# Kernel tuning notes

Measured on AMD Instinct MI355X. Metric: run time of the kernel, lower is better.

## Reference

```python
import jax, jax.numpy as jnp
import numpy as np

D_MODEL = 512
NUM_HEADS = 8
D_K = D_MODEL // NUM_HEADS


def setup_inputs() -> dict:
    key = jax.random.key(0)
    ks = jax.random.split(key, 9)
    B, N = 4, 2048
    x = jax.random.normal(ks[0], (B, N, D_MODEL), dtype=jnp.float32)
    s = 1.0 / np.sqrt(D_MODEL)
    Wq = jax.random.normal(ks[1], (D_MODEL, D_MODEL), dtype=jnp.float32) * s
    bq = jax.random.normal(ks[2], (D_MODEL,), dtype=jnp.float32) * 0.02
    Wk = jax.random.normal(ks[3], (D_MODEL, D_MODEL), dtype=jnp.float32) * s
    bk = jax.random.normal(ks[4], (D_MODEL,), dtype=jnp.float32) * 0.02
    Wv = jax.random.normal(ks[5], (D_MODEL, D_MODEL), dtype=jnp.float32) * s
    bv = jax.random.normal(ks[6], (D_MODEL,), dtype=jnp.float32) * 0.02
    Wo = jax.random.normal(ks[7], (D_MODEL, D_MODEL), dtype=jnp.float32) * s
    bo = jax.random.normal(ks[8], (D_MODEL,), dtype=jnp.float32) * 0.02
    return {"x": x, "Wq": Wq, "bq": bq, "Wk": Wk, "bk": bk,
            "Wv": Wv, "bv": bv, "Wo": Wo, "bo": bo}


def reference(x, Wq, bq, Wk, bk, Wv, bv, Wo, bo):
    B, N, _ = x.shape
    # project and split heads: [B, H, N, d_k]
    def split_heads(t):
        return t.reshape(B, N, NUM_HEADS, D_K).transpose(0, 2, 1, 3)
    Q = split_heads(x @ Wq + bq)
    K = split_heads(x @ Wk + bk)
    V = split_heads(x @ Wv + bv)
    scale = 1.0 / np.sqrt(D_K)
    scores = jnp.einsum('bhqd,bhkd->bhqk', Q, K) * scale  # [B,H,N,N]
    probs = jax.nn.softmax(scores, axis=-1)
    attn = jnp.einsum('bhqk,bhkd->bhqd', probs, V)
    attn = attn.transpose(0, 2, 1, 3).reshape(B, N, D_MODEL)
    return attn @ Wo + bo
```

## Files before the change

kernel.cpp:

```cpp
#include <hip/hip_runtime.h>
#include <math.h>

#define D_MODEL 512
#define N_SEQ   2048
#define H       8
#define DK      64

typedef __attribute__((ext_vector_type(8)))  short bf16x8;
typedef __attribute__((ext_vector_type(4)))  float f32x4;
typedef __attribute__((ext_vector_type(16))) float f32x16;

__device__ __forceinline__ unsigned short f2b(float f) {
    unsigned int u = __float_as_uint(f);
    u += 0x7FFF + ((u >> 16) & 1);
    return (unsigned short)(u >> 16);
}

__device__ __forceinline__ unsigned int pack2(float lo, float hi) {
#if __has_builtin(__builtin_amdgcn_cvt_pk_bf16_f32)
    typedef __attribute__((ext_vector_type(2))) short bf16x2;
    bf16x2 p = __builtin_amdgcn_cvt_pk_bf16_f32(lo, hi);
    return (unsigned int)(unsigned short)p[0] |
           ((unsigned int)(unsigned short)p[1] << 16);
#else
    return (unsigned int)f2b(lo) | ((unsigned int)f2b(hi) << 16);
#endif
}

__device__ __forceinline__ float fexp2(float x) {
#if __has_builtin(__builtin_amdgcn_exp2f)
    return __builtin_amdgcn_exp2f(x);
#else
    return __expf(x * 0.6931471805599453f);
#endif
}

#define SC2 0.18033688011112042f

__global__ void convert_bf16(const float* __restrict__ in,
                             unsigned short* __restrict__ out)
{
    const int i = (blockIdx.x * 256 + threadIdx.x) * 8;
    float4 a = *(const float4*)(in + i);
    float4 b = *(const float4*)(in + i + 4);
    unsigned int w[4];
    w[0] = pack2(a.x, a.y); w[1] = pack2(a.z, a.w);
    w[2] = pack2(b.x, b.y); w[3] = pack2(b.z, b.w);
    *(bf16x8*)(out + i) = *(bf16x8*)w;
}

__global__ void transpose_all(
    const float* __restrict__ W0, const float* __restrict__ W1,
    const float* __restrict__ W2, const float* __restrict__ W3,
    unsigned short* __restrict__ T0, unsigned short* __restrict__ T1,
    unsigned short* __restrict__ T2, unsigned short* __restrict__ T3)
{
    const float* W; unsigned short* Wt;
    if      (blockIdx.z == 0) { W = W0; Wt = T0; }
    else if (blockIdx.z == 1) { W = W1; Wt = T1; }
    else if (blockIdx.z == 2) { W = W2; Wt = T2; }
    else                      { W = W3; Wt = T3; }

    __shared__ float t[32][33];
    const int tx = threadIdx.x, ty = threadIdx.y;
    const int x = blockIdx.x * 32 + tx;
    const int y0 = blockIdx.y * 32;
    for (int i = ty; i < 32; i += 8)
        t[i][tx] = W[(size_t)(y0 + i) * D_MODEL + x];
    __syncthreads();
    const int ox = blockIdx.y * 32 + tx;
    const int oy0 = blockIdx.x * 32;
    for (int i = ty; i < 32; i += 8)
        Wt[(size_t)(oy0 + i) * D_MODEL + ox] = f2b(t[tx][i]);
}

__global__ __launch_bounds__(256, 4) void gemm_qkv(
    const unsigned short* __restrict__ xb,
    const unsigned short* __restrict__ Wtq,
    const unsigned short* __restrict__ Wtk,
    const unsigned short* __restrict__ Wtv,
    const float* __restrict__ bq, const float* __restrict__ bk,
    const float* __restrict__ bv,
    unsigned short* __restrict__ Qb, unsigned short* __restrict__ Kb,
    unsigned short* __restrict__ Vtb)
{
    __shared__ unsigned short As[128][72];
    __shared__ unsigned short Bs[64][72];

    const unsigned short* Wt; const float* bias; unsigned short* out; int isV;
    float sc;
    if (blockIdx.z == 0)      { Wt = Wtq; bias = bq; out = Qb;  isV = 0; sc = SC2; }
    else if (blockIdx.z == 1) { Wt = Wtk; bias = bk; out = Kb;  isV = 0; sc = 1.0f; }
    else                      { Wt = Wtv; bias = bv; out = Vtb; isV = 1; sc = 1.0f; }

    const int tid  = threadIdx.x;
    const int lane = tid & 63, wave = tid >> 6;
    const int m0 = blockIdx.y * 128, n0 = blockIdx.x * 64;
    const int wm = (wave & 1) * 64, wn = (wave >> 1) * 32;
    const int cn = lane & 15, g = lane >> 4;

    const int arow = tid >> 1, acol = (tid & 1) * 32;
    const int brow = tid >> 2, bcol = (tid & 3) * 16;
    const unsigned short* Ag = xb + (size_t)(m0 + arow) * D_MODEL + acol;
    const unsigned short* Bg = Wt + (size_t)(n0 + brow) * D_MODEL + bcol;

    f32x4 acc[4][2];
    #pragma unroll
    for (int i = 0; i < 4; ++i)
        #pragma unroll
        for (int j = 0; j < 2; ++j)
            acc[i][j] = (f32x4){0.f, 0.f, 0.f, 0.f};

    for (int k0 = 0; k0 < D_MODEL; k0 += 64) {
        bf16x8 av[4], bv2[2];
        #pragma unroll
        for (int q = 0; q < 4; ++q) av[q] = *(const bf16x8*)(Ag + k0 + q * 8);
        #pragma unroll
        for (int q = 0; q < 2; ++q) bv2[q] = *(const bf16x8*)(Bg + k0 + q * 8);
        __syncthreads();
        #pragma unroll
        for (int q = 0; q < 4; ++q) *(bf16x8*)&As[arow][acol + q * 8] = av[q];
        #pragma unroll
        for (int q = 0; q < 2; ++q) *(bf16x8*)&Bs[brow][bcol + q * 8] = bv2[q];
        __syncthreads();

        #pragma unroll
        for (int ks = 0; ks < 2; ++ks) {
            bf16x8 af[4], bf[2];
            #pragma unroll
            for (int i = 0; i < 4; ++i)
                af[i] = *(const bf16x8*)&As[wm + i * 16 + cn][ks * 32 + g * 8];
            #pragma unroll
            for (int j = 0; j < 2; ++j)
                bf[j] = *(const bf16x8*)&Bs[wn + j * 16 + cn][ks * 32 + g * 8];
            if (!isV) {
                #pragma unroll
                for (int i = 0; i < 4; ++i)
                    #pragma unroll
                    for (int j = 0; j < 2; ++j)
                        acc[i][j] = __builtin_amdgcn_mfma_f32_16x16x32_bf16(
                            bf[j], af[i], acc[i][j], 0, 0, 0);
            } else {
                #pragma unroll
                for (int i = 0; i < 4; ++i)
                    #pragma unroll
                    for (int j = 0; j < 2; ++j)
                        acc[i][j] = __builtin_amdgcn_mfma_f32_16x16x32_bf16(
                            af[i], bf[j], acc[i][j], 0, 0, 0);
            }
        }
    }

    if (!isV) {
        #pragma unroll
        for (int j = 0; j < 2; ++j) {
            const int dbase = n0 + wn + j * 16 + g * 4;
            const int hh = dbase >> 6, dd = dbase & 63;
            float4 bb = *(const float4*)&bias[dbase];
            #pragma unroll
            for (int i = 0; i < 4; ++i) {
                const int tt = m0 + wm + i * 16 + cn;
                const int bi = tt >> 11, tok = tt & (N_SEQ - 1);
                ushort4 pk;
                pk.x = f2b((acc[i][j][0] + bb.x) * sc);
                pk.y = f2b((acc[i][j][1] + bb.y) * sc);
                pk.z = f2b((acc[i][j][2] + bb.z) * sc);
                pk.w = f2b((acc[i][j][3] + bb.w) * sc);
                *(ushort4*)(out + (((size_t)bi * H + hh) * N_SEQ + tok) * DK + dd) = pk;
            }
        }
    } else {
        #pragma unroll
        for (int j = 0; j < 2; ++j) {
            const int n = n0 + wn + j * 16 + cn;
            const int hh = n >> 6, dd = n & 63;
            const float bb = bias[n];
            #pragma unroll
            for (int i = 0; i < 4; ++i) {
                const int m = m0 + wm + i * 16 + g * 4;
                const int bi = m >> 11, t = m & (N_SEQ - 1);
                ushort4 pk;
                pk.x = f2b(acc[i][j][0] + bb);
                pk.y = f2b(acc[i][j][1] + bb);
                pk.z = f2b(acc[i][j][2] + bb);
                pk.w = f2b(acc[i][j][3] + bb);
                *(ushort4*)(out + (((size_t)bi * H + hh) * DK + dd) * N_SEQ + t) = pk;
            }
        }
    }
}

__global__ __launch_bounds__(256, 4) void gemm_o(
    const unsigned short* __restrict__ A,
    const unsigned short* __restrict__ Wt,
    const float* __restrict__ bias, float* __restrict__ out)
{
    __shared__ unsigned short As[64][72];
    __shared__ unsigned short Bs[64][72];

    const int tid  = threadIdx.x;
    const int lane = tid & 63, wave = tid >> 6;
    const int m0 = blockIdx.y * 64, n0 = blockIdx.x * 64;
    const int wm = (wave & 1) * 32, wn = (wave >> 1) * 32;
    const int cn = lane & 15, g = lane >> 4;

    const int srow = tid >> 2;
    const int scol = (tid & 3) * 16;
    const unsigned short* Ag = A  + (size_t)(m0 + srow) * D_MODEL + scol;
    const unsigned short* Bg = Wt + (size_t)(n0 + srow) * D_MODEL + scol;

    f32x4 acc[2][2];
    #pragma unroll
    for (int i = 0; i < 2; ++i)
        #pragma unroll
        for (int j = 0; j < 2; ++j)
            acc[i][j] = (f32x4){0.f, 0.f, 0.f, 0.f};

    for (int k0 = 0; k0 < D_MODEL; k0 += 64) {
        bf16x8 av[2], bv[2];
        #pragma unroll
        for (int q = 0; q < 2; ++q) {
            av[q] = *(const bf16x8*)(Ag + k0 + q * 8);
            bv[q] = *(const bf16x8*)(Bg + k0 + q * 8);
        }
        __syncthreads();
        #pragma unroll
        for (int q = 0; q < 2; ++q) {
            *(bf16x8*)&As[srow][scol + q * 8] = av[q];
            *(bf16x8*)&Bs[srow][scol + q * 8] = bv[q];
        }
        __syncthreads();

        #pragma unroll
        for (int ks = 0; ks < 2; ++ks) {
            bf16x8 af[2], bf[2];
            #pragma unroll
            for (int i = 0; i < 2; ++i)
                af[i] = *(const bf16x8*)&As[wm + i * 16 + cn][ks * 32 + g * 8];
            #pragma unroll
            for (int j = 0; j < 2; ++j)
                bf[j] = *(const bf16x8*)&Bs[wn + j * 16 + cn][ks * 32 + g * 8];
            #pragma unroll
            for (int i = 0; i < 2; ++i)
                #pragma unroll
                for (int j = 0; j < 2; ++j)
                    acc[i][j] = __builtin_amdgcn_mfma_f32_16x16x32_bf16(
                        af[i], bf[j], acc[i][j], 0, 0, 0);
        }
    }

    #pragma unroll
    for (int j = 0; j < 2; ++j) {
        const int n = n0 + wn + j * 16 + cn;
        const float bb = bias[n];
        #pragma unroll
        for (int i = 0; i < 2; ++i)
            #pragma unroll
            for (int r = 0; r < 4; ++r) {
                const int m = m0 + wm + i * 16 + g * 4 + r;
                out[(size_t)m * D_MODEL + n] = acc[i][j][r] + bb;
            }
    }
}

__global__ __launch_bounds__(256, 2) void attn_mfma(
    const unsigned short* __restrict__ Q,
    const unsigned short* __restrict__ K,
    const unsigned short* __restrict__ Vt,
    unsigned short* __restrict__ ctx)
{
    __shared__ unsigned short SM[2][2][64][72];

    const int bid = blockIdx.x;
    const int qt = (bid >> 3) & 15;
    const int bh = (bid & 7) * 4 + (bid >> 7);
    const int b = bh >> 3, h = bh & 7;

    const int tid = threadIdx.x, lane = tid & 63, wave = tid >> 6;
    const int sp = wave >> 1;
    const int w4 = wave & 1;
    const int lq = lane & 31, hf = lane >> 5;
    const int qbase = qt * 128 + w4 * 64;

    const size_t hb = (size_t)b * H + h;
    const unsigned short* Qp = Q  + hb * N_SEQ * DK;
    const unsigned short* Kp = K  + hb * N_SEQ * DK;
    const unsigned short* Vp = Vt + hb * DK * N_SEQ;

    bf16x8 qf[2][4];
    #pragma unroll
    for (int u = 0; u < 2; ++u)
        #pragma unroll
        for (int kd = 0; kd < 4; ++kd)
            qf[u][kd] = *(const bf16x8*)(Qp +
                (size_t)(qbase + u * 32 + lq) * DK + kd * 16 + hf * 8);

    f32x16 O[2][2], Ol[2];
    #pragma unroll
    for (int u = 0; u < 2; ++u)
        #pragma unroll
        for (int r = 0; r < 16; ++r) {
            O[u][0][r] = 0.f; O[u][1][r] = 0.f; Ol[u][r] = 0.f;
        }

    bf16x8 onesA;
    {
        const short v = (lq == 0) ? (short)0x3F80 : (short)0;
        #pragma unroll
        for (int j = 0; j < 8; ++j) onesA[j] = v;
    }

    const int sps = tid >> 7;
    const int tl = tid & 127;
    const int krow = tl >> 1, kcol = (tl & 1) * 32;
    unsigned short (*Kss)[72] = SM[sps][0];
    unsigned short (*Vss)[72] = SM[sps][1];
    unsigned short (*Ks)[72]  = SM[sp][0];
    unsigned short (*Vs)[72]  = SM[sp][1];

    for (int it = 0; it < 16; ++it) {
        const int j0 = sps * (N_SEQ / 2) + it * 64;
        bf16x8 kv[4], vv[4];
        #pragma unroll
        for (int q = 0; q < 4; ++q) {
            kv[q] = *(const bf16x8*)(Kp + (size_t)(j0 + krow) * DK + kcol + q * 8);
            vv[q] = *(const bf16x8*)(Vp + (size_t)krow * N_SEQ + j0 + kcol + q * 8);
        }
        bf16x8 sw[4];
        {
            ushort4* v0 = (ushort4*)&vv[0]; ushort4* v1 = (ushort4*)&vv[1];
            ushort4* v2 = (ushort4*)&vv[2]; ushort4* v3 = (ushort4*)&vv[3];
            ushort4* s0 = (ushort4*)&sw[0]; ushort4* s1 = (ushort4*)&sw[1];
            ushort4* s2 = (ushort4*)&sw[2]; ushort4* s3 = (ushort4*)&sw[3];
            s0[0] = v0[0]; s0[1] = v1[0];
            s1[0] = v0[1]; s1[1] = v1[1];
            s2[0] = v2[0]; s2[1] = v3[0];
            s3[0] = v2[1]; s3[1] = v3[1];
        }
        __syncthreads();
        #pragma unroll
        for (int q = 0; q < 4; ++q) {
            *(bf16x8*)&Kss[krow][kcol + q * 8] = kv[q];
            *(bf16x8*)&Vss[krow][kcol + q * 8] = sw[q];
        }
        __syncthreads();

        bf16x8 ka0[4], ka1[4];
        #pragma unroll
        for (int kd = 0; kd < 4; ++kd) {
            ka0[kd] = *(const bf16x8*)&Ks[lq][kd * 16 + hf * 8];
            ka1[kd] = *(const bf16x8*)&Ks[32 + lq][kd * 16 + hf * 8];
        }

        unsigned int pA[2][4][2], pB[2][4][2];
        #pragma unroll
        for (int u = 0; u < 2; ++u) {
            f32x16 s0, s1;
            #pragma unroll
            for (int r = 0; r < 16; ++r) { s0[r] = 0.f; s1[r] = 0.f; }
            #pragma unroll
            for (int kd = 0; kd < 4; ++kd) {
                s0 = __builtin_amdgcn_mfma_f32_32x32x16_bf16(ka0[kd], qf[u][kd], s0, 0, 0, 0);
                s1 = __builtin_amdgcn_mfma_f32_32x32x16_bf16(ka1[kd], qf[u][kd], s1, 0, 0, 0);
            }
            #pragma unroll
            for (int c = 0; c < 4; ++c)
                #pragma unroll
                for (int p = 0; p < 2; ++p) {
                    pA[u][c][p] = pack2(fexp2(s0[4 * c + 2 * p]),
                                        fexp2(s0[4 * c + 2 * p + 1]));
                    pB[u][c][p] = pack2(fexp2(s1[4 * c + 2 * p]),
                                        fexp2(s1[4 * c + 2 * p + 1]));
                }
        }

        bf16x8 va0[4], va1[4];
        #pragma unroll
        for (int ks = 0; ks < 4; ++ks) {
            va0[ks] = *(const bf16x8*)&Vs[lq][ks * 16 + hf * 8];
            va1[ks] = *(const bf16x8*)&Vs[32 + lq][ks * 16 + hf * 8];
        }

        #pragma unroll
        for (int u = 0; u < 2; ++u)
            #pragma unroll
            for (int ks = 0; ks < 4; ++ks) {
                const unsigned int (*src)[2] = (ks < 2) ? pA[u] : pB[u];
                const int c2 = (ks & 1) * 2;
                bf16x8 bp;
                unsigned int* bpu = (unsigned int*)&bp;
                bpu[0] = src[c2][0];     bpu[1] = src[c2][1];
                bpu[2] = src[c2 + 1][0]; bpu[3] = src[c2 + 1][1];
                O[u][0] = __builtin_amdgcn_mfma_f32_32x32x16_bf16(va0[ks], bp, O[u][0], 0, 0, 0);
                O[u][1] = __builtin_amdgcn_mfma_f32_32x32x16_bf16(va1[ks], bp, O[u][1], 0, 0, 0);
                Ol[u]   = __builtin_amdgcn_mfma_f32_32x32x16_bf16(onesA,   bp, Ol[u],   0, 0, 0);
            }
    }

    float* R    = (float*)&SM[0][0][0][0];
    float* Laux = R + 2 * 2 * 64 * 32;

    __syncthreads();
    if (sp == 1) {
        #pragma unroll
        for (int u = 0; u < 2; ++u) {
            #pragma unroll
            for (int dt = 0; dt < 2; ++dt)
                #pragma unroll
                for (int r = 0; r < 16; ++r) {
                    const int d = (r & 3) + 8 * (r >> 2) + 4 * hf + 32 * dt;
                    R[(((w4 * 2 + u) * 64) + d) * 32 + lq] = O[u][dt][r];
                }
            if (hf == 0) Laux[(w4 * 2 + u) * 32 + lq] = Ol[u][0];
        }
    }
    __syncthreads();
    if (sp == 0) {
        #pragma unroll
        for (int u = 0; u < 2; ++u) {
            #pragma unroll
            for (int dt = 0; dt < 2; ++dt)
                #pragma unroll
                for (int r = 0; r < 16; ++r) {
                    const int d = (r & 3) + 8 * (r >> 2) + 4 * hf + 32 * dt;
                    O[u][dt][r] += R[(((w4 * 2 + u) * 64) + d) * 32 + lq];
                }
            const float lsum = Ol[u][0] + Laux[(w4 * 2 + u) * 32 + lq];
            const float linv = 1.0f / __shfl(lsum, lq);

            unsigned short* ob = ctx +
                ((size_t)b * N_SEQ + qbase + u * 32 + lq) * D_MODEL
                + h * DK + hf * 4;
            #pragma unroll
            for (int dt = 0; dt < 2; ++dt)
                #pragma unroll
                for (int c = 0; c < 4; ++c) {
                    unsigned int w2[2];
                    w2[0] = pack2(O[u][dt][4 * c + 0] * linv,
                                  O[u][dt][4 * c + 1] * linv);
                    w2[1] = pack2(O[u][dt][4 * c + 2] * linv,
                                  O[u][dt][4 * c + 3] * linv);
                    *(unsigned int*)(ob + dt * 32 + c * 8)     = w2[0];
                    *(unsigned int*)(ob + dt * 32 + c * 8 + 2) = w2[1];
                }
        }
    }
}

extern "C" void kernel_launch(void* const* d_in, const int* in_sizes, int n_in,
                              void* d_out, int out_size, void* d_ws, size_t ws_size,
                              hipStream_t stream)
{
    const float* x  = (const float*)d_in[0];
    const float* Wq = (const float*)d_in[1];
    const float* bq = (const float*)d_in[2];
    const float* Wk = (const float*)d_in[3];
    const float* bk = (const float*)d_in[4];
    const float* Wv = (const float*)d_in[5];
    const float* bv = (const float*)d_in[6];
    const float* Wo = (const float*)d_in[7];
    const float* bo = (const float*)d_in[8];
    float* out = (float*)d_out;

    const int M = in_sizes[0] / D_MODEL;
    const size_t NX = (size_t)M * D_MODEL;
    const size_t NW = (size_t)D_MODEL * D_MODEL;

    unsigned short* xb  = (unsigned short*)d_ws;
    unsigned short* Wtq = xb + NX;
    unsigned short* Wtk = Wtq + NW;
    unsigned short* Wtv = Wtk + NW;
    unsigned short* Wto = Wtv + NW;
    unsigned short* Qb  = Wto + NW;
    unsigned short* Kb  = Qb + NX;
    unsigned short* Vtb = Kb + NX;
    unsigned short* ctx = Vtb + NX;

    convert_bf16<<<NX / (256 * 8), 256, 0, stream>>>(x, xb);
    transpose_all<<<dim3(16, 16, 4), dim3(32, 8), 0, stream>>>(
        Wq, Wk, Wv, Wo, Wtq, Wtk, Wtv, Wto);

    gemm_qkv<<<dim3(D_MODEL / 64, M / 128, 3), 256, 0, stream>>>(
        xb, Wtq, Wtk, Wtv, bq, bk, bv, Qb, Kb, Vtb);
    attn_mfma<<<512, 256, 0, stream>>>(Qb, Kb, Vtb, ctx);
    gemm_o<<<dim3(D_MODEL / 64, M / 64), 256, 0, stream>>>(ctx, Wto, bo, out);
}
```

Before: 179.1 us.

## Drop LDS staging in projection GEMMs, load MFMA fragments directly from global

```diff
diff --git a/kernel.cpp b/kernel.cpp
--- a/kernel.cpp
+++ b/kernel.cpp
@@ -84,76 +84,61 @@
     unsigned short* __restrict__ Qb, unsigned short* __restrict__ Kb,
     unsigned short* __restrict__ Vtb)
 {
-    __shared__ unsigned short As[128][72];
-    __shared__ unsigned short Bs[64][72];
-
-    const unsigned short* Wt; const float* bias; unsigned short* out; int isV;
-    float sc;
-    if (blockIdx.z == 0)      { Wt = Wtq; bias = bq; out = Qb;  isV = 0; sc = SC2; }
-    else if (blockIdx.z == 1) { Wt = Wtk; bias = bk; out = Kb;  isV = 0; sc = 1.0f; }
-    else                      { Wt = Wtv; bias = bv; out = Vtb; isV = 1; sc = 1.0f; }
-
-    const int tid  = threadIdx.x;
-    const int lane = tid & 63, wave = tid >> 6;
-    const int m0 = blockIdx.y * 128, n0 = blockIdx.x * 64;
-    const int wm = (wave & 1) * 64, wn = (wave >> 1) * 32;
+    const int bid = blockIdx.x;
+    const int m0 = ((bid & 7) + 8 * ((bid >> 3) & 7)) * 128;
+    const int nz = bid >> 6;
+    const int n0 = (nz & 3) * 128;
+    const int z  = nz >> 2;
+
+    const unsigned short* Wt; const float* bias; unsigned short* out;
+    float sc; int isV;
+    if (z == 0)      { Wt = Wtq; bias = bq; out = Qb;  sc = SC2;  isV = 0; }
+    else if (z == 1) { Wt = Wtk; bias = bk; out = Kb;  sc = 1.0f; isV = 0; }
+    else             { Wt = Wtv; bias = bv; out = Vtb; sc = 1.0f; isV = 1; }
+
+    const int lane = threadIdx.x & 63, wave = threadIdx.x >> 6;
+    const int wm = (wave & 1) * 64, wn = (wave >> 1) * 64;
     const int cn = lane & 15, g = lane >> 4;
 
-    const int arow = tid >> 1, acol = (tid & 1) * 32;
-    const int brow = tid >> 2, bcol = (tid & 3) * 16;
-    const unsigned short* Ag = xb + (size_t)(m0 + arow) * D_MODEL + acol;
-    const unsigned short* Bg = Wt + (size_t)(n0 + brow) * D_MODEL + bcol;
-
-    f32x4 acc[4][2];
+    const unsigned short* Arow = xb + (size_t)(m0 + wm + cn) * D_MODEL + g * 8;
+    const unsigned short* Brow = Wt + (size_t)(n0 + wn + cn) * D_MODEL + g * 8;
+
+    f32x4 acc[4][4];
     #pragma unroll
     for (int i = 0; i < 4; ++i)
         #pragma unroll
-        for (int j = 0; j < 2; ++j)
+        for (int j = 0; j < 4; ++j)
             acc[i][j] = (f32x4){0.f, 0.f, 0.f, 0.f};
 
-    for (int k0 = 0; k0 < D_MODEL; k0 += 64) {
-        bf16x8 av[4], bv2[2];
-        #pragma unroll
-        for (int q = 0; q < 4; ++q) av[q] = *(const bf16x8*)(Ag + k0 + q * 8);
-        #pragma unroll
-        for (int q = 0; q < 2; ++q) bv2[q] = *(const bf16x8*)(Bg + k0 + q * 8);
-        __syncthreads();
-        #pragma unroll
-        for (int q = 0; q < 4; ++q) *(bf16x8*)&As[arow][acol + q * 8] = av[q];
-        #pragma unroll
-        for (int q = 0; q < 2; ++q) *(bf16x8*)&Bs[brow][bcol + q * 8] = bv2[q];
-        __syncthreads();
-
-        #pragma unroll
-        for (int ks = 0; ks < 2; ++ks) {
-            bf16x8 af[4], bf[2];
+    #pragma unroll 4
+    for (int k0 = 0; k0 < D_MODEL; k0 += 32) {
+        bf16x8 af[4], bf[4];
+        #pragma unroll
+        for (int i = 0; i < 4; ++i)
+            af[i] = *(const bf16x8*)(Arow + (size_t)i * 16 * D_MODEL + k0);
+        #pragma unroll
+        for (int j = 0; j < 4; ++j)
+            bf[j] = *(const bf16x8*)(Brow + (size_t)j * 16 * D_MODEL + k0);
+        if (!isV) {
             #pragma unroll
             for (int i = 0; i < 4; ++i)
-                af[i] = *(const bf16x8*)&As[wm + i * 16 + cn][ks * 32 + g * 8];
-            #pragma unroll
-            for (int j = 0; j < 2; ++j)
-                bf[j] = *(const bf16x8*)&Bs[wn + j * 16 + cn][ks * 32 + g * 8];
-            if (!isV) {
-                #pragma unroll
-                for (int i = 0; i < 4; ++i)
-                    #pragma unroll
-                    for (int j = 0; j < 2; ++j)
-                        acc[i][j] = __builtin_amdgcn_mfma_f32_16x16x32_bf16(
-                            bf[j], af[i], acc[i][j], 0, 0, 0);
-            } else {
-                #pragma unroll
-                for (int i = 0; i < 4; ++i)
-                    #pragma unroll
-                    for (int j = 0; j < 2; ++j)
-                        acc[i][j] = __builtin_amdgcn_mfma_f32_16x16x32_bf16(
-                            af[i], bf[j], acc[i][j], 0, 0, 0);
-            }
+                #pragma unroll
+                for (int j = 0; j < 4; ++j)
+                    acc[i][j] = __builtin_amdgcn_mfma_f32_16x16x32_bf16(
+                        bf[j], af[i], acc[i][j], 0, 0, 0);
+        } else {
+            #pragma unroll
+            for (int i = 0; i < 4; ++i)
+                #pragma unroll
+                for (int j = 0; j < 4; ++j)
+                    acc[i][j] = __builtin_amdgcn_mfma_f32_16x16x32_bf16(
+                        af[i], bf[j], acc[i][j], 0, 0, 0);
         }
     }
 
     if (!isV) {
         #pragma unroll
-        for (int j = 0; j < 2; ++j) {
+        for (int j = 0; j < 4; ++j) {
             const int dbase = n0 + wn + j * 16 + g * 4;
             const int hh = dbase >> 6, dd = dbase & 63;
             float4 bb = *(const float4*)&bias[dbase];
@@ -171,7 +156,7 @@
         }
     } else {
         #pragma unroll
-        for (int j = 0; j < 2; ++j) {
+        for (int j = 0; j < 4; ++j) {
             const int n = n0 + wn + j * 16 + cn;
             const int hh = n >> 6, dd = n & 63;
             const float bb = bias[n];
@@ -195,62 +180,43 @@
     const unsigned short* __restrict__ Wt,
     const float* __restrict__ bias, float* __restrict__ out)
 {
-    __shared__ unsigned short As[64][72];
-    __shared__ unsigned short Bs[64][72];
-
-    const int tid  = threadIdx.x;
-    const int lane = tid & 63, wave = tid >> 6;
-    const int m0 = blockIdx.y * 64, n0 = blockIdx.x * 64;
-    const int wm = (wave & 1) * 32, wn = (wave >> 1) * 32;
+    const int bid = blockIdx.x;
+    const int m0 = ((bid & 7) + 8 * ((bid >> 3) & 15)) * 64;
+    const int n0 = (bid >> 7) * 128;
+
+    const int lane = threadIdx.x & 63, wave = threadIdx.x >> 6;
+    const int wm = (wave & 1) * 32, wn = (wave >> 1) * 64;
     const int cn = lane & 15, g = lane >> 4;
 
-    const int srow = tid >> 2;
-    const int scol = (tid & 3) * 16;
-    const unsigned short* Ag = A  + (size_t)(m0 + srow) * D_MODEL + scol;
-    const unsigned short* Bg = Wt + (size_t)(n0 + srow) * D_MODEL + scol;
-
-    f32x4 acc[2][2];
+    const unsigned short* Arow = A  + (size_t)(m0 + wm + cn) * D_MODEL + g * 8;
+    const unsigned short* Brow = Wt + (size_t)(n0 + wn + cn) * D_MODEL + g * 8;
+
+    f32x4 acc[2][4];
     #pragma unroll
     for (int i = 0; i < 2; ++i)
         #pragma unroll
-        for (int j = 0; j < 2; ++j)
+        for (int j = 0; j < 4; ++j)
             acc[i][j] = (f32x4){0.f, 0.f, 0.f, 0.f};
 
-    for (int k0 = 0; k0 < D_MODEL; k0 += 64) {
-        bf16x8 av[2], bv[2];
-        #pragma unroll
-        for (int q = 0; q < 2; ++q) {
-            av[q] = *(const bf16x8*)(Ag + k0 + q * 8);
-            bv[q] = *(const bf16x8*)(Bg + k0 + q * 8);
-        }
-        __syncthreads();
-        #pragma unroll
-        for (int q = 0; q < 2; ++q) {
-            *(bf16x8*)&As[srow][scol + q * 8] = av[q];
-            *(bf16x8*)&Bs[srow][scol + q * 8] = bv[q];
-        }
-        __syncthreads();
-
-        #pragma unroll
-        for (int ks = 0; ks < 2; ++ks) {
-            bf16x8 af[2], bf[2];
-            #pragma unroll
-            for (int i = 0; i < 2; ++i)
-                af[i] = *(const bf16x8*)&As[wm + i * 16 + cn][ks * 32 + g * 8];
-            #pragma unroll
-            for (int j = 0; j < 2; ++j)
-                bf[j] = *(const bf16x8*)&Bs[wn + j * 16 + cn][ks * 32 + g * 8];
-            #pragma unroll
-            for (int i = 0; i < 2; ++i)
-                #pragma unroll
-                for (int j = 0; j < 2; ++j)
-                    acc[i][j] = __builtin_amdgcn_mfma_f32_16x16x32_bf16(
-                        af[i], bf[j], acc[i][j], 0, 0, 0);
-        }
+    #pragma unroll 4
+    for (int k0 = 0; k0 < D_MODEL; k0 += 32) {
+        bf16x8 af[2], bf[4];
+        #pragma unroll
+        for (int i = 0; i < 2; ++i)
+            af[i] = *(const bf16x8*)(Arow + (size_t)i * 16 * D_MODEL + k0);
+        #pragma unroll
+        for (int j = 0; j < 4; ++j)
+            bf[j] = *(const bf16x8*)(Brow + (size_t)j * 16 * D_MODEL + k0);
+        #pragma unroll
+        for (int i = 0; i < 2; ++i)
+            #pragma unroll
+            for (int j = 0; j < 4; ++j)
+                acc[i][j] = __builtin_amdgcn_mfma_f32_16x16x32_bf16(
+                    af[i], bf[j], acc[i][j], 0, 0, 0);
     }
 
     #pragma unroll
-    for (int j = 0; j < 2; ++j) {
+    for (int j = 0; j < 4; ++j) {
         const int n = n0 + wn + j * 16 + cn;
         const float bb = bias[n];
         #pragma unroll
@@ -480,8 +446,8 @@
     transpose_all<<<dim3(16, 16, 4), dim3(32, 8), 0, stream>>>(
         Wq, Wk, Wv, Wo, Wtq, Wtk, Wtv, Wto);
 
-    gemm_qkv<<<dim3(D_MODEL / 64, M / 128, 3), 256, 0, stream>>>(
+    gemm_qkv<<<768, 256, 0, stream>>>(
         xb, Wtq, Wtk, Wtv, bq, bk, bv, Qb, Kb, Vtb);
     attn_mfma<<<512, 256, 0, stream>>>(Qb, Kb, Vtb, ctx);
-    gemm_o<<<dim3(D_MODEL / 64, M / 64), 256, 0, stream>>>(ctx, Wto, bo, out);
-}
+    gemm_o<<<512, 256, 0, stream>>>(ctx, Wto, bo, out);
+}
```

New measurement: 266.3 us. 1.49x slower.
